# Kernel tuning notes

Hardware: AMD Instinct MI355X
Metric: run time of the kernel (lower is better)

## Reference

```python
import jax, jax.numpy as jnp
import numpy as np

OMEGA = 30.0

def _conv1x1(x, W, b):
    # x: [B, Cin, D, H, W]; W: [Cout, Cin]; b: [Cout]
    return jnp.einsum('oi,bidhw->bodhw', W, x) + b[None, :, None, None, None]

def setup_inputs() -> dict:
    key = jax.random.key(0)
    ks = jax.random.split(key, 12)
    B, D, H, Wd = 1, 8, 128, 128
    C = 256
    shp = (B, 3, D, H, Wd)
    std = np.sqrt(6.0 / C) / OMEGA
    return {
        'z': jax.random.normal(ks[0], shp, jnp.float32),
        'n': jax.random.normal(ks[1], shp, jnp.float32),
        'ad': jax.random.normal(ks[2], shp, jnp.float32),
        's': jax.random.normal(ks[3], shp, jnp.float32),
        'pixel_coords': jax.random.uniform(ks[4], shp, jnp.float32),
        'view_direction': jax.random.normal(ks[5], shp, jnp.float32),
        'W1': jax.random.normal(ks[6], (C, 12), jnp.float32) * std,
        'b1': jax.random.normal(ks[7], (C,), jnp.float32) * std,
        'W2': jax.random.normal(ks[8], (C, C), jnp.float32) * std,
        'b2': jax.random.normal(ks[9], (C,), jnp.float32) * std,
        'W4': jax.random.normal(ks[10], (3, C), jnp.float32) * 1e-4,
        'b4': jax.random.normal(ks[11], (3,), jnp.float32) * 1e-4,
    }

def reference(z, n, ad, s, pixel_coords, view_direction, W1, b1, W2, b2, W4, b4):
    # concat along channel dim: [B, 12, D, H, W]
    x = jnp.concatenate((s, n, pixel_coords, view_direction), axis=1)
    h = jnp.sin(OMEGA * _conv1x1(x, W1, b1))
    h = jnp.sin(OMEGA * _conv1x1(h, W2, b2))
    s_out = 0.5 * jnp.sin(OMEGA * _conv1x1(h, W4, b4))
    # lighting_predict_mode == 'total'
    return z + s_out
```

## Files before the change

### kernel.cpp

```cpp
#include <hip/hip_runtime.h>
#include <hip/hip_bf16.h>

#define NPIX (8*128*128)
#define CH   256

typedef __attribute__((ext_vector_type(8))) short bf16x8;
typedef __attribute__((ext_vector_type(4))) float f32x4;

__device__ inline unsigned int pkbf(float a, float b) {
    union { __hip_bfloat162 h; unsigned int u; } c;
    c.h = __float22bfloat162_rn(float2{a, b});
    return c.u;
}
__device__ inline unsigned short f2bf(float f) {
    unsigned int u = __float_as_uint(f);
    return (unsigned short)((u + 0x7FFFu + ((u >> 16) & 1u)) >> 16);
}
__device__ inline int kperm32(int k) {
    return (k & ~31) | ((k & 15) << 1) | ((k >> 4) & 1);
}

__global__ __launch_bounds__(256) void conv_weights(
    const float* __restrict__ W1, const float* __restrict__ W2,
    const float* __restrict__ W4,
    unsigned short* __restrict__ W2b, unsigned short* __restrict__ W1b,
    unsigned short* __restrict__ W4b)
{
    if (blockIdx.x < 256) {
        const int o = blockIdx.x, k = threadIdx.x;
        W2b[o*CH + kperm32(k)] = f2bf(W2[o*CH + k]);
    } else {
        const int t = threadIdx.x;
        #pragma unroll
        for (int j = 0; j < 16; ++j)
            W1b[t*16 + j] = (j < 12) ? f2bf(W1[t*12 + j]) : (unsigned short)0;
        const int kp = kperm32(t);
        #pragma unroll
        for (int r = 0; r < 16; ++r)
            W4b[r*CH + kp] = (r < 3) ? f2bf(W4[r*CH + t]) : (unsigned short)0;
    }
}

template<bool PRE>
__global__ __launch_bounds__(512, 4) void rendernet3(
    const float* __restrict__ z,
    const float* __restrict__ nrm,
    const float* __restrict__ sph,
    const float* __restrict__ pc,
    const float* __restrict__ vd,
    const float* __restrict__ W1,
    const float* __restrict__ b1,
    const float* __restrict__ W2f,
    const unsigned short* __restrict__ W2b,
    const unsigned short* __restrict__ W1b,
    const float* __restrict__ b2,
    const float* __restrict__ W4f,
    const unsigned short* __restrict__ W4b,
    const float* __restrict__ b4,
    float* __restrict__ out)
{
    __shared__ __align__(16) char smem[64*512 + 64*80];
    char* xb = smem + 64*512;

    const int tid     = threadIdx.x;
    const int lane    = tid & 63;
    const int wave    = tid >> 6;
    const int lm      = lane & 15;
    const int lg      = lane >> 4;
    const int n0      = wave * 32;
    const int pixbase = blockIdx.x * 64;

    f32x4 acc[4][2];

    if constexpr (PRE) {
        {
            const int gp = pixbase + lane;
            unsigned int w0 = 0u, w1 = 0u;
            if (wave == 0) {
                w0 = pkbf(sph[0*NPIX+gp], sph[1*NPIX+gp]);
                w1 = pkbf(sph[2*NPIX+gp], nrm[0*NPIX+gp]);
            } else if (wave == 1) {
                w0 = pkbf(nrm[1*NPIX+gp], nrm[2*NPIX+gp]);
                w1 = pkbf(pc [0*NPIX+gp], pc [1*NPIX+gp]);
            } else if (wave == 2) {
                w0 = pkbf(pc[2*NPIX+gp], vd[0*NPIX+gp]);
                w1 = pkbf(vd[1*NPIX+gp], vd[2*NPIX+gp]);
            }
            *(unsigned int*)(xb + lane*80 + wave*8)     = w0;
            *(unsigned int*)(xb + lane*80 + wave*8 + 4) = w1;
        }
        __syncthreads();

        #pragma unroll
        for (int nf = 0; nf < 2; ++nf) {
            const float bv = b1[n0 + nf*16 + lm];
            #pragma unroll
            for (int mf = 0; mf < 4; ++mf) acc[mf][nf] = (f32x4){bv, bv, bv, bv};
        }

        bf16x8 w1f[2];
        #pragma unroll
        for (int nf = 0; nf < 2; ++nf) {
            bf16x8 t = *(const bf16x8*)(W1b + (n0 + nf*16 + lm)*16 + (lg & 1)*8);
            w1f[nf] = (lg < 2) ? t : (bf16x8){0,0,0,0,0,0,0,0};
        }
        bf16x8 ax[4];
        #pragma unroll
        for (int mf = 0; mf < 4; ++mf)
            ax[mf] = *(const bf16x8*)(xb + (mf*16 + lm)*80 + lg*16);

        #pragma unroll
        for (int nf = 0; nf < 2; ++nf)
            #pragma unroll
            for (int mf = 0; mf < 4; ++mf)
                acc[mf][nf] = __builtin_amdgcn_mfma_f32_16x16x32_bf16(
                                  ax[mf], w1f[nf], acc[mf][nf], 0, 0, 0);

        #pragma unroll
        for (int mf = 0; mf < 4; ++mf)
            #pragma unroll
            for (int r = 0; r < 4; ++r) {
                const int pix = mf*16 + lg*4 + r;
                const unsigned int pk = pkbf(__sinf(30.0f*acc[mf][0][r]),
                                             __sinf(30.0f*acc[mf][1][r]));
                *(unsigned int*)(smem + pix*512 + ((n0*2 + lm*4) ^ ((pix & 31) << 4))) = pk;
            }
    } else {
        const int gp = pixbase + lane;
        float xv[12];
        #pragma unroll
        for (int k = 0; k < 3; ++k) xv[k]     = sph[k*NPIX + gp];
        #pragma unroll
        for (int k = 0; k < 3; ++k) xv[3 + k] = nrm[k*NPIX + gp];
        #pragma unroll
        for (int k = 0; k < 3; ++k) xv[6 + k] = pc [k*NPIX + gp];
        #pragma unroll
        for (int k = 0; k < 3; ++k) xv[9 + k] = vd [k*NPIX + gp];
        #pragma unroll
        for (int c = 0; c < 32; ++c) {
            const int cc = n0 + c;
            float a = b1[cc];
            #pragma unroll
            for (int k = 0; k < 12; ++k) a += W1[cc*12 + k] * xv[k];
            const int kp = n0 + ((c & 15) << 1) + (c >> 4);
            *(unsigned short*)(smem + lane*512 + ((kp*2) ^ ((lane & 31) << 4))) =
                f2bf(__sinf(30.0f * a));
        }
    }
    __syncthreads();

    #pragma unroll
    for (int nf = 0; nf < 2; ++nf) {
        const float bv = b2[n0 + nf*16 + lm];
        #pragma unroll
        for (int mf = 0; mf < 4; ++mf) acc[mf][nf] = (f32x4){bv, bv, bv, bv};
    }

    if constexpr (PRE) {
        const unsigned short* bp = W2b + (n0 + lm)*CH + lg*8;
        #pragma unroll
        for (int k0i = 0; k0i < 8; ++k0i) {
            bf16x8 bfr[2];
            #pragma unroll
            for (int nf = 0; nf < 2; ++nf)
                bfr[nf] = *(const bf16x8*)(bp + nf*16*CH + k0i*32);
            bf16x8 afr[4];
            #pragma unroll
            for (int mf = 0; mf < 4; ++mf) {
                const int pr = mf*16 + lm;
                afr[mf] = *(const bf16x8*)(smem + pr*512 +
                              ((k0i*64 + lg*16) ^ ((pr & 31) << 4)));
            }
            #pragma unroll
            for (int nf = 0; nf < 2; ++nf)
                #pragma unroll
                for (int mf = 0; mf < 4; ++mf)
                    acc[mf][nf] = __builtin_amdgcn_mfma_f32_16x16x32_bf16(
                                      afr[mf], bfr[nf], acc[mf][nf], 0, 0, 0);
        }
    } else {
        #pragma unroll
        for (int k0i = 0; k0i < 8; ++k0i) {
            bf16x8 afr[4];
            #pragma unroll
            for (int mf = 0; mf < 4; ++mf) {
                const int pr = mf*16 + lm;
                afr[mf] = *(const bf16x8*)(smem + pr*512 +
                              ((k0i*64 + lg*16) ^ ((pr & 31) << 4)));
            }
            #pragma unroll
            for (int nf = 0; nf < 2; ++nf) {
                bf16x8 t;
                #pragma unroll
                for (int j = 0; j < 8; ++j) {
                    const int kp = k0i*32 + lg*8 + j;
                    const int kr = (kp & ~31) | ((kp & 1) << 4) | ((kp >> 1) & 15);
                    t[j] = (short)f2bf(W2f[(n0 + nf*16 + lm)*CH + kr]);
                }
                #pragma unroll
                for (int mf = 0; mf < 4; ++mf)
                    acc[mf][nf] = __builtin_amdgcn_mfma_f32_16x16x32_bf16(
                                      afr[mf], t, acc[mf][nf], 0, 0, 0);
            }
        }
    }
    __syncthreads();

    #pragma unroll
    for (int mf = 0; mf < 4; ++mf)
        #pragma unroll
        for (int r = 0; r < 4; ++r) {
            const int pix = mf*16 + lg*4 + r;
            const unsigned int pk = pkbf(__sinf(30.0f*acc[mf][0][r]),
                                         __sinf(30.0f*acc[mf][1][r]));
            *(unsigned int*)(smem + pix*512 + ((n0*2 + lm*4) ^ ((pix & 31) << 4))) = pk;
        }
    __syncthreads();

    if (wave == 0) {
        const float b4v = (lm < 3) ? b4[lm] : 0.0f;
        f32x4 d[4];
        #pragma unroll
        for (int mf = 0; mf < 4; ++mf) d[mf] = (f32x4){b4v, b4v, b4v, b4v};

        #pragma unroll
        for (int k0i = 0; k0i < 8; ++k0i) {
            bf16x8 b4f;
            if constexpr (PRE) {
                b4f = *(const bf16x8*)(W4b + lm*CH + k0i*32 + lg*8);
            } else {
                #pragma unroll
                for (int j = 0; j < 8; ++j) {
                    const int kp = k0i*32 + lg*8 + j;
                    const int kr = (kp & ~31) | ((kp & 1) << 4) | ((kp >> 1) & 15);
                    b4f[j] = (lm < 3) ? (short)f2bf(W4f[lm*CH + kr]) : (short)0;
                }
            }
            bf16x8 afr[4];
            #pragma unroll
            for (int mf = 0; mf < 4; ++mf) {
                const int pr = mf*16 + lm;
                afr[mf] = *(const bf16x8*)(smem + pr*512 +
                              ((k0i*64 + lg*16) ^ ((pr & 31) << 4)));
            }
            #pragma unroll
            for (int mf = 0; mf < 4; ++mf)
                d[mf] = __builtin_amdgcn_mfma_f32_16x16x32_bf16(
                            afr[mf], b4f, d[mf], 0, 0, 0);
        }

        if (lm < 3) {
            #pragma unroll
            for (int mf = 0; mf < 4; ++mf)
                #pragma unroll
                for (int r = 0; r < 4; ++r) {
                    const int pix = mf*16 + lg*4 + r;
                    const int gi  = lm*NPIX + pixbase + pix;
                    out[gi] = z[gi] + 0.5f * __sinf(30.0f * d[mf][r]);
                }
        }
    }
}

extern "C" void kernel_launch(void* const* d_in, const int* in_sizes, int n_in,
                              void* d_out, int out_size, void* d_ws, size_t ws_size,
                              hipStream_t stream) {
    const float* z   = (const float*)d_in[0];
    const float* nrm = (const float*)d_in[1];
    const float* s   = (const float*)d_in[3];
    const float* pc  = (const float*)d_in[4];
    const float* vd  = (const float*)d_in[5];
    const float* W1  = (const float*)d_in[6];
    const float* b1  = (const float*)d_in[7];
    const float* W2  = (const float*)d_in[8];
    const float* b2  = (const float*)d_in[9];
    const float* W4  = (const float*)d_in[10];
    const float* b4  = (const float*)d_in[11];
    float* out = (float*)d_out;

    const size_t need = (size_t)(CH*CH + 16*CH + 16*CH) * sizeof(unsigned short);
    if (ws_size >= need) {
        unsigned short* W2b = (unsigned short*)d_ws;
        unsigned short* W1b = W2b + CH*CH;
        unsigned short* W4b = W1b + 16*CH;
        conv_weights<<<dim3(257), dim3(256), 0, stream>>>(W1, W2, W4, W2b, W1b, W4b);
        rendernet3<true><<<dim3(NPIX/64), dim3(512), 0, stream>>>(
            z, nrm, s, pc, vd, W1, b1, W2, W2b, W1b, b2, W4, W4b, b4, out);
    } else {
        rendernet3<false><<<dim3(NPIX/64), dim3(512), 0, stream>>>(
            z, nrm, s, pc, vd, W1, b1, W2, nullptr, nullptr, b2, W4, nullptr, b4, out);
    }
}
```

Measured before the change: 125.3 us.

## Split final layer across all waves with LDS reduction and prefetch W2 into registers

The last 256->3 layer, previously computed by wave 0 alone over eight K steps, is now split so each of the eight waves handles one 32-wide K slice, with partial sums reduced through shared memory. The W2 bf16 fragments and the z values are loaded into registers at kernel start so their latency overlaps the first layer. This shortens the serial tail and hides global loads, but it adds 64 registers of W2 fragments per thread and lowers the occupancy hint from 4 to 3 blocks, plus an extra barrier.

```diff
diff --git a/kernel.cpp b/kernel.cpp
--- a/kernel.cpp
+++ b/kernel.cpp
@@ -42,7 +42,7 @@
 }
 
 template<bool PRE>
-__global__ __launch_bounds__(512, 4) void rendernet3(
+__global__ __launch_bounds__(512, 3) void rendernet4(
     const float* __restrict__ z,
     const float* __restrict__ nrm,
     const float* __restrict__ sph,
@@ -59,8 +59,9 @@
     const float* __restrict__ b4,
     float* __restrict__ out)
 {
-    __shared__ __align__(16) char smem[64*512 + 64*80];
-    char* xb = smem + 64*512;
+    __shared__ __align__(16) char smem[64*512 + 6144];
+    char*  xb    = smem + 64*512;
+    float* red_f = (float*)(smem + 64*512);
 
     const int tid     = threadIdx.x;
     const int lane    = tid & 63;
@@ -69,6 +70,19 @@
     const int lg      = lane >> 4;
     const int n0      = wave * 32;
     const int pixbase = blockIdx.x * 64;
+
+    float zv = 0.0f;
+    if (tid < 192) zv = z[(tid >> 6)*NPIX + pixbase + (tid & 63)];
+
+    bf16x8 w2r[16];
+    if constexpr (PRE) {
+        const unsigned short* bp = W2b + (n0 + lm)*CH + lg*8;
+        #pragma unroll
+        for (int k0i = 0; k0i < 8; ++k0i)
+            #pragma unroll
+            for (int nf = 0; nf < 2; ++nf)
+                w2r[k0i*2 + nf] = *(const bf16x8*)(bp + nf*16*CH + k0i*32);
+    }
 
     f32x4 acc[4][2];
 
@@ -157,13 +171,8 @@
     }
 
     if constexpr (PRE) {
-        const unsigned short* bp = W2b + (n0 + lm)*CH + lg*8;
         #pragma unroll
         for (int k0i = 0; k0i < 8; ++k0i) {
-            bf16x8 bfr[2];
-            #pragma unroll
-            for (int nf = 0; nf < 2; ++nf)
-                bfr[nf] = *(const bf16x8*)(bp + nf*16*CH + k0i*32);
             bf16x8 afr[4];
             #pragma unroll
             for (int mf = 0; mf < 4; ++mf) {
@@ -176,7 +185,7 @@
                 #pragma unroll
                 for (int mf = 0; mf < 4; ++mf)
                     acc[mf][nf] = __builtin_amdgcn_mfma_f32_16x16x32_bf16(
-                                      afr[mf], bfr[nf], acc[mf][nf], 0, 0, 0);
+                                      afr[mf], w2r[k0i*2 + nf], acc[mf][nf], 0, 0, 0);
         }
     } else {
         #pragma unroll
@@ -217,37 +226,32 @@
         }
     __syncthreads();
 
-    if (wave == 0) {
-        const float b4v = (lm < 3) ? b4[lm] : 0.0f;
+    {
+        bf16x8 b4f;
+        if constexpr (PRE) {
+            b4f = *(const bf16x8*)(W4b + lm*CH + wave*32 + lg*8);
+        } else {
+            #pragma unroll
+            for (int j = 0; j < 8; ++j) {
+                const int kp = wave*32 + lg*8 + j;
+                const int kr = (kp & ~31) | ((kp & 1) << 4) | ((kp >> 1) & 15);
+                b4f[j] = (lm < 3) ? (short)f2bf(W4f[lm*CH + kr]) : (short)0;
+            }
+        }
         f32x4 d[4];
         #pragma unroll
-        for (int mf = 0; mf < 4; ++mf) d[mf] = (f32x4){b4v, b4v, b4v, b4v};
-
-        #pragma unroll
-        for (int k0i = 0; k0i < 8; ++k0i) {
-            bf16x8 b4f;
-            if constexpr (PRE) {
-                b4f = *(const bf16x8*)(W4b + lm*CH + k0i*32 + lg*8);
-            } else {
-                #pragma unroll
-                for (int j = 0; j < 8; ++j) {
-                    const int kp = k0i*32 + lg*8 + j;
-                    const int kr = (kp & ~31) | ((kp & 1) << 4) | ((kp >> 1) & 15);
-                    b4f[j] = (lm < 3) ? (short)f2bf(W4f[lm*CH + kr]) : (short)0;
-                }
-            }
-            bf16x8 afr[4];
-            #pragma unroll
-            for (int mf = 0; mf < 4; ++mf) {
-                const int pr = mf*16 + lm;
-                afr[mf] = *(const bf16x8*)(smem + pr*512 +
-                              ((k0i*64 + lg*16) ^ ((pr & 31) << 4)));
-            }
-            #pragma unroll
-            for (int mf = 0; mf < 4; ++mf)
-                d[mf] = __builtin_amdgcn_mfma_f32_16x16x32_bf16(
-                            afr[mf], b4f, d[mf], 0, 0, 0);
-        }
+        for (int mf = 0; mf < 4; ++mf) d[mf] = (f32x4){0.f, 0.f, 0.f, 0.f};
+
+        bf16x8 afr[4];
+        #pragma unroll
+        for (int mf = 0; mf < 4; ++mf) {
+            const int pr = mf*16 + lm;
+            afr[mf] = *(const bf16x8*)(smem + pr*512 +
+                          ((wave*64 + lg*16) ^ ((pr & 31) << 4)));
+        }
+        #pragma unroll
+        for (int mf = 0; mf < 4; ++mf)
+            d[mf] = __builtin_amdgcn_mfma_f32_16x16x32_bf16(afr[mf], b4f, d[mf], 0, 0, 0);
 
         if (lm < 3) {
             #pragma unroll
@@ -255,10 +259,18 @@
                 #pragma unroll
                 for (int r = 0; r < 4; ++r) {
                     const int pix = mf*16 + lg*4 + r;
-                    const int gi  = lm*NPIX + pixbase + pix;
-                    out[gi] = z[gi] + 0.5f * __sinf(30.0f * d[mf][r]);
+                    red_f[wave*192 + lm*64 + pix] = d[mf][r];
                 }
         }
+    }
+    __syncthreads();
+
+    if (tid < 192) {
+        float t = 0.f;
+        #pragma unroll
+        for (int w = 0; w < 8; ++w) t += red_f[w*192 + tid];
+        const int c3 = tid >> 6, p = tid & 63;
+        out[c3*NPIX + pixbase + p] = zv + 0.5f * __sinf(30.0f * (t + b4[c3]));
     }
 }
 
@@ -284,10 +296,10 @@
         unsigned short* W1b = W2b + CH*CH;
         unsigned short* W4b = W1b + 16*CH;
         conv_weights<<<dim3(257), dim3(256), 0, stream>>>(W1, W2, W4, W2b, W1b, W4b);
-        rendernet3<true><<<dim3(NPIX/64), dim3(512), 0, stream>>>(
+        rendernet4<true><<<dim3(NPIX/64), dim3(512), 0, stream>>>(
             z, nrm, s, pc, vd, W1, b1, W2, W2b, W1b, b2, W4, W4b, b4, out);
     } else {
-        rendernet3<false><<<dim3(NPIX/64), dim3(512), 0, stream>>>(
+        rendernet4<false><<<dim3(NPIX/64), dim3(512), 0, stream>>>(
             z, nrm, s, pc, vd, W1, b1, W2, nullptr, nullptr, b2, W4, nullptr, b4, out);
     }
 }
```

Result: slower. 142.2 us (+13.5%).
